# Optimization experiments

Hardware: AMD Instinct MI355X
Metric: run time of the kernel (lower is better)

Reference implementation:

```python
import jax, jax.numpy as jnp
import numpy as np

HIDDEN = 1024
NUM_HEADS = 16
HEAD_DIM = HIDDEN // NUM_HEADS
GRID_SIZE = 5
SPLINE_ORDER = 3
NUM_COEF = GRID_SIZE + SPLINE_ORDER  # 8


def make_grid(in_features):
    # efficient-kan default grid: range [-1, 1], extended by spline_order on each side
    h = 2.0 / GRID_SIZE
    g = jnp.arange(-SPLINE_ORDER, GRID_SIZE + SPLINE_ORDER + 1, dtype=jnp.float32) * h - 1.0
    return jnp.broadcast_to(g, (in_features, g.shape[0]))  # (in, G+2k+1)


def b_splines(x, grid):
    # x: (N, in); grid: (in, G+2k+1) -> bases (N, in, G+k)
    x = x[..., None]
    bases = ((x >= grid[:, :-1]) & (x < grid[:, 1:])).astype(x.dtype)
    for k in range(1, SPLINE_ORDER + 1):
        left = (x - grid[:, : -(k + 1)]) / (grid[:, k:-1] - grid[:, : -(k + 1)])
        right = (grid[:, k + 1 :] - x) / (grid[:, k + 1 :] - grid[:, 1:-k])
        bases = left * bases[..., :-1] + right * bases[..., 1:]
    return bases


def kan_linear(x, base_w, spline_w, spline_scaler):
    # x: (..., in); base_w: (out, in); spline_w: (out, in, C); spline_scaler: (out, in)
    in_f = x.shape[-1]
    x2 = x.reshape(-1, in_f)
    base = jax.nn.silu(x2) @ base_w.T
    bases = b_splines(x2, make_grid(in_f))                      # (N, in, C)
    sw = spline_w * spline_scaler[..., None]                    # (out, in, C)
    spline = bases.reshape(x2.shape[0], -1) @ sw.reshape(sw.shape[0], -1).T
    return (base + spline).reshape(*x.shape[:-1], base_w.shape[0])


def apply_rope(x):
    # x: (B, H, S, D); interleaved rotary (lucidrains convention), theta=10000
    d, s = x.shape[-1], x.shape[-2]
    inv_freq = 1.0 / (10000.0 ** (jnp.arange(0, d, 2, dtype=jnp.float32) / d))
    freqs = jnp.arange(s, dtype=jnp.float32)[:, None] * inv_freq[None, :]  # (S, d/2)
    cos = jnp.repeat(jnp.cos(freqs), 2, axis=-1)
    sin = jnp.repeat(jnp.sin(freqs), 2, axis=-1)
    x1, x2 = x[..., 0::2], x[..., 1::2]
    rot = jnp.stack((-x2, x1), axis=-1).reshape(x.shape)
    return x * cos + rot * sin


def setup_inputs() -> dict:
    key = jax.random.key(0)
    ks = jax.random.split(key, 10)
    B, S, H = 2, 2048, HIDDEN
    H3 = 3 * H
    scale = 0.02
    return {
        "q": jax.random.normal(ks[0], (B, S, H), jnp.float32),
        "k": jax.random.normal(ks[1], (B, S, H), jnp.float32),
        "v": jax.random.normal(ks[2], (B, S, H), jnp.float32),
        "attn_mask": jnp.zeros((S, S), jnp.float32),
        "qkv_base_w": jax.random.normal(ks[3], (H3, H3), jnp.float32) * scale,
        "qkv_spline_w": jax.random.normal(ks[4], (H3, H3, NUM_COEF), jnp.float32) * scale,
        "qkv_scaler": jnp.ones((H3, H3), jnp.float32),
        "out_base_w": jax.random.normal(ks[5], (H, H), jnp.float32) * scale,
        "out_spline_w": jax.random.normal(ks[6], (H, H, NUM_COEF), jnp.float32) * scale,
        "out_scaler": jnp.ones((H, H), jnp.float32),
    }


def reference(q, k, v, attn_mask, qkv_base_w, qkv_spline_w, qkv_scaler,
              out_base_w, out_spline_w, out_scaler):
    B, S, H = q.shape
    x = jnp.concatenate((q, k, v), axis=2)                       # (B, S, 3H)
    qkv = kan_linear(x, qkv_base_w, qkv_spline_w, qkv_scaler)    # (B, S, 3H)
    qkv = qkv.reshape(B, S, NUM_HEADS, 3 * HEAD_DIM).transpose(0, 2, 1, 3)
    queries, keys, values = jnp.split(qkv, 3, axis=-1)           # each (B, nh, S, hd)
    queries = apply_rope(queries)
    keys = apply_rope(keys)
    scores = jnp.einsum("bhqd,bhkd->bhqk", queries, keys) / (HEAD_DIM ** 0.5) + attn_mask
    attention = jax.nn.softmax(scores, axis=-1)
    context = jnp.einsum("bhqk,bhkd->bhqd", attention, values)
    context = context.transpose(0, 2, 1, 3).reshape(B, S, H)
    return kan_linear(context, out_base_w, out_spline_w, out_scaler)
```

## Files before the change

### kernel.cpp

```cpp
#include <hip/hip_runtime.h>
#include <hip/hip_bf16.h>
#include <stdint.h>

typedef __bf16 bf16;
typedef __attribute__((ext_vector_type(4))) __bf16 bf16x4;
typedef __attribute__((ext_vector_type(8))) __bf16 bf16x8;
typedef __attribute__((ext_vector_type(4))) float f32x4;

#define DEVI __device__ __forceinline__

constexpr int BATCH = 2, SEQ = 2048, HID = 1024, NHEAD = 16, HDIM = 64;
constexpr int H3 = 3072;
constexpr int MROWS = BATCH * SEQ;
constexpr int KEXP = 9;
constexpr int K1DIM = H3 * KEXP;
constexpr int K2DIM = HID * KEXP;

constexpr size_t WQ_OFF  = 0;
constexpr size_t AQ_OFF  = 169869312;
constexpr size_t CQ_OFF  = AQ_OFF + 226492416;
constexpr size_t QR_OFF  = CQ_OFF + 50331648;
constexpr size_t KR_OFF  = QR_OFF + 8388608;
constexpr size_t VB_OFF  = KR_OFF + 8388608;
constexpr size_t CTX_OFF = VB_OFF + 8388608;
constexpr size_t A2_OFF  = 0;
constexpr size_t W2_OFF  = 75497472;
constexpr size_t MB_OFF  = W2_OFF + 18874368;

DEVI void gld_lds16(const void* g, void* l) {
  __builtin_amdgcn_global_load_lds((const __attribute__((address_space(1))) void*)g,
                                   (__attribute__((address_space(3))) void*)l, 16, 0, 0);
}

#define WAITVM0() asm volatile("s_waitcnt vmcnt(0)" ::: "memory")
#define MEMFENCE() asm volatile("" ::: "memory")
#define BARRIER() do { __builtin_amdgcn_s_barrier(); asm volatile("" ::: "memory"); } while (0)

DEVI void silu_bases(float x, float* o9) {
  o9[0] = x / (1.0f + __expf(-x));
  float g[12];
#pragma unroll
  for (int j = 0; j < 12; ++j) g[j] = (float)(j - 3) * 0.4f - 1.0f;
  float b[11];
#pragma unroll
  for (int j = 0; j < 11; ++j) b[j] = (x >= g[j] && x < g[j + 1]) ? 1.0f : 0.0f;
#pragma unroll
  for (int k = 1; k <= 3; ++k) {
    const float inv = (k == 1) ? 2.5f : (k == 2) ? 1.25f : (1.0f / 1.2f);
#pragma unroll
    for (int j = 0; j + k < 11; ++j) {
      b[j] = (x - g[j]) * inv * b[j] + (g[j + k + 1] - x) * inv * b[j + 1];
    }
  }
#pragma unroll
  for (int c = 0; c < 8; ++c) o9[1 + c] = b[c];
}

__global__ __launch_bounds__(256)
void wprep_kernel(const float* __restrict__ bw, const float* __restrict__ sw,
                  const float* __restrict__ sc, bf16* __restrict__ W, int KK) {
  __shared__ bf16 buf[256 * KEXP];
  const int tid = threadIdx.x;
  const int n = blockIdx.y;
  const int i0 = blockIdx.x * 256;
  const size_t idx = (size_t)n * KK + i0 + tid;
  float base = bw[idx];
  float scal = sc[idx];
  const float4* sp = (const float4*)(sw + idx * 8);
  float4 s0 = sp[0], s1 = sp[1];
  bf16* o = buf + tid * KEXP;
  o[0] = (bf16)base;
  o[1] = (bf16)(s0.x * scal); o[2] = (bf16)(s0.y * scal);
  o[3] = (bf16)(s0.z * scal); o[4] = (bf16)(s0.w * scal);
  o[5] = (bf16)(s1.x * scal); o[6] = (bf16)(s1.y * scal);
  o[7] = (bf16)(s1.z * scal); o[8] = (bf16)(s1.w * scal);
  __syncthreads();
  bf16* dst = W + (size_t)n * KK * KEXP + (size_t)i0 * KEXP;
#pragma unroll
  for (int j = tid; j < 256 * KEXP / 8; j += 256)
    *(bf16x8*)(dst + j * 8) = *(const bf16x8*)(buf + j * 8);
}

__global__ __launch_bounds__(256)
void act_qkv_kernel(const float* __restrict__ qin, const float* __restrict__ kin,
                    const float* __restrict__ vin, bf16* __restrict__ A) {
  __shared__ bf16 buf[256 * KEXP];
  const int tid = threadIdx.x;
  const int m = blockIdx.y;
  const int i0 = blockIdx.x * 256;
  const int i = i0 + tid;
  const int which = i >> 10, off = i & 1023;
  const float* src = (which == 0) ? qin : (which == 1) ? kin : vin;
  float x = src[(size_t)m * HID + off];
  float o9[9];
  silu_bases(x, o9);
  bf16* o = buf + tid * KEXP;
#pragma unroll
  for (int c = 0; c < 9; ++c) o[c] = (bf16)o9[c];
  __syncthreads();
  bf16* dst = A + (size_t)m * K1DIM + (size_t)i0 * KEXP;
#pragma unroll
  for (int j = tid; j < 256 * KEXP / 8; j += 256)
    *(bf16x8*)(dst + j * 8) = *(const bf16x8*)(buf + j * 8);
}

__global__ __launch_bounds__(256)
void act_out_kernel(const float* __restrict__ ctx, bf16* __restrict__ A) {
  __shared__ bf16 buf[256 * KEXP];
  const int tid = threadIdx.x;
  const int m = blockIdx.y;
  const int i0 = blockIdx.x * 256;
  float x = ctx[(size_t)m * HID + i0 + tid];
  float o9[9];
  silu_bases(x, o9);
  bf16* o = buf + tid * KEXP;
#pragma unroll
  for (int c = 0; c < 9; ++c) o[c] = (bf16)o9[c];
  __syncthreads();
  bf16* dst = A + (size_t)m * K2DIM + (size_t)i0 * KEXP;
#pragma unroll
  for (int j = tid; j < 256 * KEXP / 8; j += 256)
    *(bf16x8*)(dst + j * 8) = *(const bf16x8*)(buf + j * 8);
}

__global__ __launch_bounds__(256)
void maskprep_kernel(const float* __restrict__ m, bf16* __restrict__ mb) {
  int i = (blockIdx.x * 256 + threadIdx.x) * 4;
  float4 v = *(const float4*)(m + i);
  bf16x4 o = { (bf16)v.x, (bf16)v.y, (bf16)v.z, (bf16)v.w };
  *(bf16x4*)(mb + i) = o;
}

__global__ __launch_bounds__(256, 2)
void gemm_kernel(const bf16* __restrict__ A, const bf16* __restrict__ Bw,
                 float* __restrict__ C, int N, int K) {
  __shared__ bf16 As[128 * 64];
  __shared__ bf16 Bs[128 * 64];
  const int tid = threadIdx.x;
  const int lane = tid & 63;
  const int l15 = lane & 15, lq = lane >> 4;
  const int wid = tid >> 6;
  const int wm = (wid >> 1) * 64, wn = (wid & 1) * 64;
  const int bm = blockIdx.y, bn = blockIdx.x;
  f32x4 acc[4][4] = {};
  const int srow = tid >> 3;
  const int schk = (tid & 7) ^ (srow & 7);
  const bf16* aB = A + (size_t)(bm * 128 + srow) * K + schk * 8;
  const bf16* bB = Bw + (size_t)(bn * 128 + srow) * K + schk * 8;

  int aoff[2][4], boff[2][4];
#pragma unroll
  for (int ks = 0; ks < 2; ++ks) {
#pragma unroll
    for (int f = 0; f < 4; ++f) {
      int arow = wm + f * 16 + l15;
      int brow = wn + f * 16 + l15;
      aoff[ks][f] = arow * 64 + (((ks * 4 + lq) ^ (arow & 7)) * 8);
      boff[ks][f] = brow * 64 + (((ks * 4 + lq) ^ (brow & 7)) * 8);
    }
  }

  for (int kt = 0; kt < K; kt += 64) {
#pragma unroll
    for (int r = 0; r < 4; ++r) {
      gld_lds16(aB + (size_t)(r * 32) * K + kt, As + r * 2048 + tid * 8);
      gld_lds16(bB + (size_t)(r * 32) * K + kt, Bs + r * 2048 + tid * 8);
    }
    __syncthreads();
#pragma unroll
    for (int ks = 0; ks < 2; ++ks) {
      bf16x8 af[4], bfr[4];
#pragma unroll
      for (int mf = 0; mf < 4; ++mf)
        af[mf] = *(const bf16x8*)&As[aoff[ks][mf]];
#pragma unroll
      for (int nf = 0; nf < 4; ++nf)
        bfr[nf] = *(const bf16x8*)&Bs[boff[ks][nf]];
#pragma unroll
      for (int mf = 0; mf < 4; ++mf)
#pragma unroll
        for (int nf = 0; nf < 4; ++nf)
          acc[mf][nf] = __builtin_amdgcn_mfma_f32_16x16x32_bf16(af[mf], bfr[nf], acc[mf][nf], 0, 0, 0);
    }
    __syncthreads();
  }
#pragma unroll
  for (int mf = 0; mf < 4; ++mf)
#pragma unroll
    for (int nf = 0; nf < 4; ++nf)
#pragma unroll
      for (int r = 0; r < 4; ++r) {
        int row = bm * 128 + wm + mf * 16 + lq * 4 + r;
        int col = bn * 128 + wn + nf * 16 + l15;
        C[(size_t)row * N + col] = acc[mf][nf][r];
      }
}

__global__ __launch_bounds__(256, 2)
void gemm2_kernel(const bf16* __restrict__ A, const bf16* __restrict__ Bw,
                  float* __restrict__ C, int N, int K) {
  __shared__ bf16 As[64 * 64];
  __shared__ bf16 Bs[128 * 64];
  const int tid = threadIdx.x;
  const int lane = tid & 63;
  const int l15 = lane & 15, lq = lane >> 4;
  const int wid = tid >> 6;
  const int wr = wid >> 1, wc = wid & 1;
  const int bm = blockIdx.y, bn = blockIdx.x;
  f32x4 acc[2][4] = {};
  const int srow = tid >> 3;
  const int schk = (tid & 7) ^ (srow & 7);
  const bf16* aB = A + (size_t)(bm * 64 + srow) * K + schk * 8;
  const bf16* bB = Bw + (size_t)(bn * 128 + srow) * K + schk * 8;

  int aoff[2][2], boff[2][4];
#pragma unroll
  for (int ks = 0; ks < 2; ++ks) {
#pragma unroll
    for (int f = 0; f < 2; ++f) {
      int arow = wr * 32 + f * 16 + l15;
      aoff[ks][f] = arow * 64 + (((ks * 4 + lq) ^ (arow & 7)) * 8);
    }
#pragma unroll
    for (int f = 0; f < 4; ++f) {
      int brow = wc * 64 + f * 16 + l15;
      boff[ks][f] = brow * 64 + (((ks * 4 + lq) ^ (brow & 7)) * 8);
    }
  }

  for (int kt = 0; kt < K; kt += 64) {
#pragma unroll
    for (int r = 0; r < 2; ++r)
      gld_lds16(aB + (size_t)(r * 32) * K + kt, As + r * 2048 + tid * 8);
#pragma unroll
    for (int r = 0; r < 4; ++r)
      gld_lds16(bB + (size_t)(r * 32) * K + kt, Bs + r * 2048 + tid * 8);
    __syncthreads();
#pragma unroll
    for (int ks = 0; ks < 2; ++ks) {
      bf16x8 af[2], bfr[4];
#pragma unroll
      for (int mf = 0; mf < 2; ++mf)
        af[mf] = *(const bf16x8*)&As[aoff[ks][mf]];
#pragma unroll
      for (int nf = 0; nf < 4; ++nf)
        bfr[nf] = *(const bf16x8*)&Bs[boff[ks][nf]];
#pragma unroll
      for (int mf = 0; mf < 2; ++mf)
#pragma unroll
        for (int nf = 0; nf < 4; ++nf)
          acc[mf][nf] = __builtin_amdgcn_mfma_f32_16x16x32_bf16(af[mf], bfr[nf], acc[mf][nf], 0, 0, 0);
    }
    __syncthreads();
  }
#pragma unroll
  for (int mf = 0; mf < 2; ++mf)
#pragma unroll
    for (int nf = 0; nf < 4; ++nf)
#pragma unroll
      for (int r = 0; r < 4; ++r) {
        int row = bm * 64 + wr * 32 + mf * 16 + lq * 4 + r;
        int col = bn * 128 + wc * 64 + nf * 16 + l15;
        C[(size_t)row * N + col] = acc[mf][nf][r];
      }
}

__global__ void rope_kernel(const float* __restrict__ Cq, bf16* __restrict__ qr,
                            bf16* __restrict__ kr, bf16* __restrict__ vt) {
  int idx = blockIdx.x * blockDim.x + threadIdx.x;
  int p = idx & 31;
  int h = (idx >> 5) & 15;
  int m = idx >> 9;
  int s = m & (SEQ - 1);
  int b = m >> 11;
  const float* row = Cq + (size_t)m * H3 + h * 192;
  float q0 = row[2 * p], q1 = row[2 * p + 1];
  float k0 = row[64 + 2 * p], k1 = row[64 + 2 * p + 1];
  float v0 = row[128 + 2 * p], v1 = row[128 + 2 * p + 1];
  float invf = expf(-(float)p * (9.210340371976184f / 32.0f));
  float fr = (float)s * invf;
  float sn, cs;
  sincosf(fr, &sn, &cs);
  const int bh = b * NHEAD + h;
  size_t o = ((size_t)bh * SEQ + s) * 64 + 2 * p;
  qr[o] = (bf16)((q0 * cs - q1 * sn) * 0.125f);
  qr[o + 1] = (bf16)((q1 * cs + q0 * sn) * 0.125f);
  kr[o] = (bf16)(k0 * cs - k1 * sn); kr[o + 1] = (bf16)(k1 * cs + k0 * sn);
  vt[((size_t)bh * 64 + 2 * p) * SEQ + s] = (bf16)v0;
  vt[((size_t)bh * 64 + 2 * p + 1) * SEQ + s] = (bf16)v1;
}

__global__ __launch_bounds__(256, 2)
void attn_kernel(const bf16* __restrict__ qr, const bf16* __restrict__ kr,
                 const bf16* __restrict__ vt, const bf16* __restrict__ maskb,
                 float* __restrict__ ctx) {
  __shared__ bf16 Kt[2][64 * 64];
  __shared__ bf16 Vt[2][64 * 64];
  __shared__ bf16 Pl[4][16 * 64];
  const int tid = threadIdx.x, lane = tid & 63, wid = tid >> 6;
  const int l15 = lane & 15, lq = lane >> 4;
  const int qt = blockIdx.x, bh = blockIdx.y;
  const int b = bh >> 4, hh = bh & 15;
  const size_t baseQ = ((size_t)bh * SEQ + qt * 64 + wid * 16) * 64;
  bf16x8 aq[2];
  aq[0] = *(const bf16x8*)&qr[baseQ + (size_t)l15 * 64 + 0 + lq * 8];
  aq[1] = *(const bf16x8*)&qr[baseQ + (size_t)l15 * 64 + 32 + lq * 8];
  float mrow[4], lrow[4];
  f32x4 oacc[4] = {};
#pragma unroll
  for (int r = 0; r < 4; ++r) { mrow[r] = -1e30f; lrow[r] = 0.0f; }
  const int srow = tid >> 3;
  const int schk = (tid & 7) ^ (srow & 7);
  const bf16* kBase = kr + ((size_t)bh * SEQ + srow) * 64 + schk * 8;
  const bf16* vBase = vt + ((size_t)bh * 64 + srow) * SEQ + schk * 8;

#define ASTAGE(bi_, kv_)                                                        \
  do {                                                                          \
    gld_lds16(kBase + (size_t)(kv_) * 64, &Kt[bi_][0] + tid * 8);               \
    gld_lds16(kBase + (size_t)((kv_) + 32) * 64, &Kt[bi_][0] + 2048 + tid * 8); \
    gld_lds16(vBase + (kv_), &Vt[bi_][0] + tid * 8);                            \
    gld_lds16(vBase + (size_t)32 * SEQ + (kv_), &Vt[bi_][0] + 2048 + tid * 8);  \
  } while (0)

  ASTAGE(0, 0);
  WAITVM0();
  BARRIER();
  for (int kv0 = 0; kv0 < SEQ; kv0 += 64) {
    const int cur = (kv0 >> 6) & 1;
    if (kv0 + 64 < SEQ) { ASTAGE(cur ^ 1, kv0 + 64); MEMFENCE(); }
    const bf16* kt = &Kt[cur][0];
    const bf16* vtl = &Vt[cur][0];
    f32x4 sacc[4] = {};
    __builtin_amdgcn_s_setprio(1);
#pragma unroll
    for (int k0 = 0; k0 < 2; ++k0) {
#pragma unroll
      for (int nf = 0; nf < 4; ++nf) {
        bf16x8 bk = *(const bf16x8*)&kt[(nf * 16 + l15) * 64 + (((k0 * 4 + lq) ^ (l15 & 7)) << 3)];
        sacc[nf] = __builtin_amdgcn_mfma_f32_16x16x32_bf16(aq[k0], bk, sacc[nf], 0, 0, 0);
      }
    }
    __builtin_amdgcn_s_setprio(0);
    const int qg0 = qt * 64 + wid * 16 + lq * 4;
#pragma unroll
    for (int nf = 0; nf < 4; ++nf) {
      int kvg = kv0 + nf * 16 + l15;
#pragma unroll
      for (int r = 0; r < 4; ++r)
        sacc[nf][r] += (float)maskb[(size_t)(qg0 + r) * SEQ + kvg];
    }
    float fac[4];
#pragma unroll
    for (int r = 0; r < 4; ++r) {
      float v = fmaxf(fmaxf(sacc[0][r], sacc[1][r]), fmaxf(sacc[2][r], sacc[3][r]));
      v = fmaxf(v, __shfl_xor(v, 1));
      v = fmaxf(v, __shfl_xor(v, 2));
      v = fmaxf(v, __shfl_xor(v, 4));
      v = fmaxf(v, __shfl_xor(v, 8));
      float mnew = fmaxf(mrow[r], v);
      fac[r] = __expf(mrow[r] - mnew);
      mrow[r] = mnew;
    }
    float rs[4] = {0, 0, 0, 0};
#pragma unroll
    for (int nf = 0; nf < 4; ++nf)
#pragma unroll
      for (int r = 0; r < 4; ++r) {
        float pv = __expf(sacc[nf][r] - mrow[r]);
        sacc[nf][r] = pv;
        rs[r] += pv;
      }
#pragma unroll
    for (int r = 0; r < 4; ++r) {
      float v = rs[r];
      v += __shfl_xor(v, 1); v += __shfl_xor(v, 2);
      v += __shfl_xor(v, 4); v += __shfl_xor(v, 8);
      lrow[r] = lrow[r] * fac[r] + v;
    }
#pragma unroll
    for (int nf = 0; nf < 4; ++nf)
#pragma unroll
      for (int r = 0; r < 4; ++r) {
        int qrow = lq * 4 + r;
        int col = nf * 16 + l15;
        Pl[wid][qrow * 64 + ((((col >> 3) ^ (qrow & 7))) << 3) + (col & 7)] = (bf16)sacc[nf][r];
      }
#pragma unroll
    for (int nf = 0; nf < 4; ++nf)
#pragma unroll
      for (int r = 0; r < 4; ++r)
        oacc[nf][r] *= fac[r];
    __builtin_amdgcn_s_setprio(1);
#pragma unroll
    for (int k0 = 0; k0 < 2; ++k0) {
      bf16x8 ap = *(const bf16x8*)&Pl[wid][l15 * 64 + (((k0 * 4 + lq) ^ (l15 & 7)) << 3)];
#pragma unroll
      for (int nf = 0; nf < 4; ++nf) {
        bf16x8 bv = *(const bf16x8*)&vtl[(nf * 16 + l15) * 64 + (((k0 * 4 + lq) ^ (l15 & 7)) << 3)];
        oacc[nf] = __builtin_amdgcn_mfma_f32_16x16x32_bf16(ap, bv, oacc[nf], 0, 0, 0);
      }
    }
    __builtin_amdgcn_s_setprio(0);
    WAITVM0();
    BARRIER();
  }
#undef ASTAGE
#pragma unroll
  for (int nf = 0; nf < 4; ++nf)
#pragma unroll
    for (int r = 0; r < 4; ++r) {
      int row = qt * 64 + wid * 16 + lq * 4 + r;
      int col = hh * 64 + nf * 16 + l15;
      ctx[((size_t)b * SEQ + row) * HID + col] = oacc[nf][r] / lrow[r];
    }
}

extern "C" void kernel_launch(void* const* d_in, const int* in_sizes, int n_in,
                              void* d_out, int out_size, void* d_ws, size_t ws_size,
                              hipStream_t stream) {
  const float* qin    = (const float*)d_in[0];
  const float* kin    = (const float*)d_in[1];
  const float* vin    = (const float*)d_in[2];
  const float* mask   = (const float*)d_in[3];
  const float* qkv_bw = (const float*)d_in[4];
  const float* qkv_sw = (const float*)d_in[5];
  const float* qkv_sc = (const float*)d_in[6];
  const float* out_bw = (const float*)d_in[7];
  const float* out_sw = (const float*)d_in[8];
  const float* out_sc = (const float*)d_in[9];
  char* ws = (char*)d_ws;
  bf16* Wq  = (bf16*)(ws + WQ_OFF);
  bf16* Aq  = (bf16*)(ws + AQ_OFF);
  float* Cq = (float*)(ws + CQ_OFF);
  bf16* qr  = (bf16*)(ws + QR_OFF);
  bf16* kr  = (bf16*)(ws + KR_OFF);
  bf16* vt  = (bf16*)(ws + VB_OFF);
  float* ctx = (float*)(ws + CTX_OFF);
  bf16* A2  = (bf16*)(ws + A2_OFF);
  bf16* W2  = (bf16*)(ws + W2_OFF);
  bf16* mb  = (bf16*)(ws + MB_OFF);

  wprep_kernel<<<dim3(H3 / 256, H3), 256, 0, stream>>>(qkv_bw, qkv_sw, qkv_sc, Wq, H3);
  act_qkv_kernel<<<dim3(H3 / 256, MROWS), 256, 0, stream>>>(qin, kin, vin, Aq);
  gemm_kernel<<<dim3(H3 / 128, MROWS / 128), 256, 0, stream>>>(Aq, Wq, Cq, H3, K1DIM);
  maskprep_kernel<<<(SEQ * SEQ) / 1024, 256, 0, stream>>>(mask, mb);
  rope_kernel<<<(MROWS * NHEAD * 32) / 256, 256, 0, stream>>>(Cq, qr, kr, vt);
  attn_kernel<<<dim3(SEQ / 64, BATCH * NHEAD), 256, 0, stream>>>(qr, kr, vt, mb, ctx);
  act_out_kernel<<<dim3(HID / 256, MROWS), 256, 0, stream>>>(ctx, A2);
  wprep_kernel<<<dim3(HID / 256, HID), 256, 0, stream>>>(out_bw, out_sw, out_sc, W2, HID);
  gemm2_kernel<<<dim3(HID / 128, MROWS / 64), 256, 0, stream>>>(A2, W2, (float*)d_out, HID, K2DIM);
}
```

Measured before the change: 1.119 ms.

## Process two 16-row query groups per wave in attention kernel

Each wave now handles 32 query rows (two 16-row groups) instead of 16, so every block covers 128 queries and the grid halves. Each K/V tile staged in shared memory is reused for twice as many queries, which halves global K/V traffic and staging per query. In exchange, register pressure rises from the doubled accumulators and the grid has fewer blocks (512), which may lower occupancy and latency hiding. The attention kernel is only part of a pipeline dominated by large KAN GEMMs.

```diff
diff --git a/kernel.cpp b/kernel.cpp
--- a/kernel.cpp
+++ b/kernel.cpp
@@ -296,19 +296,24 @@
                  float* __restrict__ ctx) {
   __shared__ bf16 Kt[2][64 * 64];
   __shared__ bf16 Vt[2][64 * 64];
-  __shared__ bf16 Pl[4][16 * 64];
+  __shared__ bf16 Pl[4][32 * 64];
   const int tid = threadIdx.x, lane = tid & 63, wid = tid >> 6;
   const int l15 = lane & 15, lq = lane >> 4;
   const int qt = blockIdx.x, bh = blockIdx.y;
   const int b = bh >> 4, hh = bh & 15;
-  const size_t baseQ = ((size_t)bh * SEQ + qt * 64 + wid * 16) * 64;
-  bf16x8 aq[2];
-  aq[0] = *(const bf16x8*)&qr[baseQ + (size_t)l15 * 64 + 0 + lq * 8];
-  aq[1] = *(const bf16x8*)&qr[baseQ + (size_t)l15 * 64 + 32 + lq * 8];
-  float mrow[4], lrow[4];
-  f32x4 oacc[4] = {};
-#pragma unroll
-  for (int r = 0; r < 4; ++r) { mrow[r] = -1e30f; lrow[r] = 0.0f; }
+  bf16x8 aq[2][2];
+#pragma unroll
+  for (int g = 0; g < 2; ++g) {
+    const size_t baseQ = ((size_t)bh * SEQ + qt * 128 + wid * 32 + g * 16) * 64;
+    aq[g][0] = *(const bf16x8*)&qr[baseQ + (size_t)l15 * 64 + 0 + lq * 8];
+    aq[g][1] = *(const bf16x8*)&qr[baseQ + (size_t)l15 * 64 + 32 + lq * 8];
+  }
+  float mrow[2][4], lrow[2][4];
+  f32x4 oacc[2][4] = {};
+#pragma unroll
+  for (int g = 0; g < 2; ++g)
+#pragma unroll
+    for (int r = 0; r < 4; ++r) { mrow[g][r] = -1e30f; lrow[g][r] = 0.0f; }
   const int srow = tid >> 3;
   const int schk = (tid & 7) ^ (srow & 7);
   const bf16* kBase = kr + ((size_t)bh * SEQ + srow) * 64 + schk * 8;
@@ -330,74 +335,82 @@
     if (kv0 + 64 < SEQ) { ASTAGE(cur ^ 1, kv0 + 64); MEMFENCE(); }
     const bf16* kt = &Kt[cur][0];
     const bf16* vtl = &Vt[cur][0];
-    f32x4 sacc[4] = {};
+    f32x4 sacc[2][4] = {};
     __builtin_amdgcn_s_setprio(1);
 #pragma unroll
     for (int k0 = 0; k0 < 2; ++k0) {
 #pragma unroll
       for (int nf = 0; nf < 4; ++nf) {
         bf16x8 bk = *(const bf16x8*)&kt[(nf * 16 + l15) * 64 + (((k0 * 4 + lq) ^ (l15 & 7)) << 3)];
-        sacc[nf] = __builtin_amdgcn_mfma_f32_16x16x32_bf16(aq[k0], bk, sacc[nf], 0, 0, 0);
+#pragma unroll
+        for (int g = 0; g < 2; ++g)
+          sacc[g][nf] = __builtin_amdgcn_mfma_f32_16x16x32_bf16(aq[g][k0], bk, sacc[g][nf], 0, 0, 0);
       }
     }
     __builtin_amdgcn_s_setprio(0);
-    const int qg0 = qt * 64 + wid * 16 + lq * 4;
-#pragma unroll
-    for (int nf = 0; nf < 4; ++nf) {
-      int kvg = kv0 + nf * 16 + l15;
-#pragma unroll
-      for (int r = 0; r < 4; ++r)
-        sacc[nf][r] += (float)maskb[(size_t)(qg0 + r) * SEQ + kvg];
-    }
-    float fac[4];
-#pragma unroll
-    for (int r = 0; r < 4; ++r) {
-      float v = fmaxf(fmaxf(sacc[0][r], sacc[1][r]), fmaxf(sacc[2][r], sacc[3][r]));
-      v = fmaxf(v, __shfl_xor(v, 1));
-      v = fmaxf(v, __shfl_xor(v, 2));
-      v = fmaxf(v, __shfl_xor(v, 4));
-      v = fmaxf(v, __shfl_xor(v, 8));
-      float mnew = fmaxf(mrow[r], v);
-      fac[r] = __expf(mrow[r] - mnew);
-      mrow[r] = mnew;
-    }
-    float rs[4] = {0, 0, 0, 0};
-#pragma unroll
-    for (int nf = 0; nf < 4; ++nf)
+#pragma unroll
+    for (int g = 0; g < 2; ++g) {
+      const int qg0 = qt * 128 + wid * 32 + g * 16 + lq * 4;
+#pragma unroll
+      for (int nf = 0; nf < 4; ++nf) {
+        int kvg = kv0 + nf * 16 + l15;
+#pragma unroll
+        for (int r = 0; r < 4; ++r)
+          sacc[g][nf][r] += (float)maskb[(size_t)(qg0 + r) * SEQ + kvg];
+      }
+      float fac[4];
 #pragma unroll
       for (int r = 0; r < 4; ++r) {
-        float pv = __expf(sacc[nf][r] - mrow[r]);
-        sacc[nf][r] = pv;
-        rs[r] += pv;
-      }
-#pragma unroll
-    for (int r = 0; r < 4; ++r) {
-      float v = rs[r];
-      v += __shfl_xor(v, 1); v += __shfl_xor(v, 2);
-      v += __shfl_xor(v, 4); v += __shfl_xor(v, 8);
-      lrow[r] = lrow[r] * fac[r] + v;
-    }
-#pragma unroll
-    for (int nf = 0; nf < 4; ++nf)
+        float v = fmaxf(fmaxf(sacc[g][0][r], sacc[g][1][r]), fmaxf(sacc[g][2][r], sacc[g][3][r]));
+        v = fmaxf(v, __shfl_xor(v, 1));
+        v = fmaxf(v, __shfl_xor(v, 2));
+        v = fmaxf(v, __shfl_xor(v, 4));
+        v = fmaxf(v, __shfl_xor(v, 8));
+        float mnew = fmaxf(mrow[g][r], v);
+        fac[r] = __expf(mrow[g][r] - mnew);
+        mrow[g][r] = mnew;
+      }
+      float rs[4] = {0, 0, 0, 0};
+#pragma unroll
+      for (int nf = 0; nf < 4; ++nf)
+#pragma unroll
+        for (int r = 0; r < 4; ++r) {
+          float pv = __expf(sacc[g][nf][r] - mrow[g][r]);
+          sacc[g][nf][r] = pv;
+          rs[r] += pv;
+        }
 #pragma unroll
       for (int r = 0; r < 4; ++r) {
-        int qrow = lq * 4 + r;
-        int col = nf * 16 + l15;
-        Pl[wid][qrow * 64 + ((((col >> 3) ^ (qrow & 7))) << 3) + (col & 7)] = (bf16)sacc[nf][r];
-      }
-#pragma unroll
-    for (int nf = 0; nf < 4; ++nf)
-#pragma unroll
-      for (int r = 0; r < 4; ++r)
-        oacc[nf][r] *= fac[r];
+        float v = rs[r];
+        v += __shfl_xor(v, 1); v += __shfl_xor(v, 2);
+        v += __shfl_xor(v, 4); v += __shfl_xor(v, 8);
+        lrow[g][r] = lrow[g][r] * fac[r] + v;
+      }
+#pragma unroll
+      for (int nf = 0; nf < 4; ++nf)
+#pragma unroll
+        for (int r = 0; r < 4; ++r) {
+          int qrow = g * 16 + lq * 4 + r;
+          int col = nf * 16 + l15;
+          Pl[wid][qrow * 64 + ((((col >> 3) ^ (qrow & 7))) << 3) + (col & 7)] = (bf16)sacc[g][nf][r];
+        }
+#pragma unroll
+      for (int nf = 0; nf < 4; ++nf)
+#pragma unroll
+        for (int r = 0; r < 4; ++r)
+          oacc[g][nf][r] *= fac[r];
+    }
     __builtin_amdgcn_s_setprio(1);
 #pragma unroll
     for (int k0 = 0; k0 < 2; ++k0) {
-      bf16x8 ap = *(const bf16x8*)&Pl[wid][l15 * 64 + (((k0 * 4 + lq) ^ (l15 & 7)) << 3)];
-#pragma unroll
-      for (int nf = 0; nf < 4; ++nf) {
-        bf16x8 bv = *(const bf16x8*)&vtl[(nf * 16 + l15) * 64 + (((k0 * 4 + lq) ^ (l15 & 7)) << 3)];
-        oacc[nf] = __builtin_amdgcn_mfma_f32_16x16x32_bf16(ap, bv, oacc[nf], 0, 0, 0);
+#pragma unroll
+      for (int g = 0; g < 2; ++g) {
+        bf16x8 ap = *(const bf16x8*)&Pl[wid][(g * 16 + l15) * 64 + (((k0 * 4 + lq) ^ (l15 & 7)) << 3)];
+#pragma unroll
+        for (int nf = 0; nf < 4; ++nf) {
+          bf16x8 bv = *(const bf16x8*)&vtl[(nf * 16 + l15) * 64 + (((k0 * 4 + lq) ^ (l15 & 7)) << 3)];
+          oacc[g][nf] = __builtin_amdgcn_mfma_f32_16x16x32_bf16(ap, bv, oacc[g][nf], 0, 0, 0);
+        }
       }
     }
     __builtin_amdgcn_s_setprio(0);
@@ -406,13 +419,15 @@
   }
 #undef ASTAGE
 #pragma unroll
-  for (int nf = 0; nf < 4; ++nf)
-#pragma unroll
-    for (int r = 0; r < 4; ++r) {
-      int row = qt * 64 + wid * 16 + lq * 4 + r;
-      int col = hh * 64 + nf * 16 + l15;
-      ctx[((size_t)b * SEQ + row) * HID + col] = oacc[nf][r] / lrow[r];
-    }
+  for (int g = 0; g < 2; ++g)
+#pragma unroll
+    for (int nf = 0; nf < 4; ++nf)
+#pragma unroll
+      for (int r = 0; r < 4; ++r) {
+        int row = qt * 128 + wid * 32 + g * 16 + lq * 4 + r;
+        int col = hh * 64 + nf * 16 + l15;
+        ctx[((size_t)b * SEQ + row) * HID + col] = oacc[g][nf][r] / lrow[g][r];
+      }
 }
 
 extern "C" void kernel_launch(void* const* d_in, const int* in_sizes, int n_in,
@@ -445,7 +460,7 @@
   gemm_kernel<<<dim3(H3 / 128, MROWS / 128), 256, 0, stream>>>(Aq, Wq, Cq, H3, K1DIM);
   maskprep_kernel<<<(SEQ * SEQ) / 1024, 256, 0, stream>>>(mask, mb);
   rope_kernel<<<(MROWS * NHEAD * 32) / 256, 256, 0, stream>>>(Cq, qr, kr, vt);
-  attn_kernel<<<dim3(SEQ / 64, BATCH * NHEAD), 256, 0, stream>>>(qr, kr, vt, mb, ctx);
+  attn_kernel<<<dim3(SEQ / 128, BATCH * NHEAD), 256, 0, stream>>>(qr, kr, vt, mb, ctx);
   act_out_kernel<<<dim3(HID / 256, MROWS), 256, 0, stream>>>(ctx, A2);
   wprep_kernel<<<dim3(HID / 256, HID), 256, 0, stream>>>(out_bw, out_sw, out_sc, W2, HID);
   gemm2_kernel<<<dim3(HID / 128, MROWS / 64), 256, 0, stream>>>(A2, W2, (float*)d_out, HID, K2DIM);
```

New measurement: 1.204 ms. 1.08x slower.

## Fuse RoPE and head split into QKV GEMM epilogue, add V transpose kernel

Applied to the files above, without the earlier changes.

The QKV GEMM epilogue now applies rotary embedding and writes bf16 q/k (q pre-scaled) and a row-major bf16 V directly, using a precomputed cos/sin table and a lane shuffle to fetch the paired element. A separate small kernel transposes V through LDS into the layout attention expects. This removes the 50MB fp32 intermediate write and readback plus the strided scatter in the old rope kernel. In exchange it adds per-element index math and scattered 2-byte stores in the epilogue, and two extra small launches.

```diff
diff --git a/kernel.cpp b/kernel.cpp
--- a/kernel.cpp
+++ b/kernel.cpp
@@ -19,6 +19,8 @@
 constexpr size_t WQ_OFF  = 0;
 constexpr size_t AQ_OFF  = 169869312;
 constexpr size_t CQ_OFF  = AQ_OFF + 226492416;
+constexpr size_t VR_OFF  = CQ_OFF;
+constexpr size_t TC_OFF  = CQ_OFF + 16777216;
 constexpr size_t QR_OFF  = CQ_OFF + 50331648;
 constexpr size_t KR_OFF  = QR_OFF + 8388608;
 constexpr size_t VB_OFF  = KR_OFF + 8388608;
@@ -54,6 +56,16 @@
   }
 #pragma unroll
   for (int c = 0; c < 8; ++c) o9[1 + c] = b[c];
+}
+
+__global__ __launch_bounds__(256)
+void tprep_kernel(float2* __restrict__ tcs) {
+  int idx = blockIdx.x * 256 + threadIdx.x;
+  int s = idx >> 5, p = idx & 31;
+  float invf = __expf(-(float)p * (9.210340371976184f / 32.0f));
+  float sn, cs;
+  __sincosf((float)s * invf, &sn, &cs);
+  tcs[idx] = make_float2(cs, sn);
 }
 
 __global__ __launch_bounds__(256)
@@ -132,8 +144,9 @@
 }
 
 __global__ __launch_bounds__(256, 2)
-void gemm_kernel(const bf16* __restrict__ A, const bf16* __restrict__ Bw,
-                 float* __restrict__ C, int N, int K) {
+void gemm1_kernel(const bf16* __restrict__ A, const bf16* __restrict__ Bw,
+                  bf16* __restrict__ qr, bf16* __restrict__ kr,
+                  bf16* __restrict__ vrow, const float2* __restrict__ tcs, int K) {
   __shared__ bf16 As[128 * 64];
   __shared__ bf16 Bs[128 * 64];
   const int tid = threadIdx.x;
@@ -184,16 +197,56 @@
     }
     __syncthreads();
   }
+
 #pragma unroll
   for (int mf = 0; mf < 4; ++mf)
 #pragma unroll
     for (int nf = 0; nf < 4; ++nf)
 #pragma unroll
-      for (int r = 0; r < 4; ++r) {
-        int row = bm * 128 + wm + mf * 16 + lq * 4 + r;
+      for (int rr = 0; rr < 4; ++rr) {
+        int row = bm * 128 + wm + mf * 16 + lq * 4 + rr;
         int col = bn * 128 + wn + nf * 16 + l15;
-        C[(size_t)row * N + col] = acc[mf][nf][r];
-      }
+        int s = row & (SEQ - 1);
+        int bb = row >> 11;
+        int h = col / 192;
+        int r2 = col - h * 192;
+        int bh = bb * NHEAD + h;
+        float val = acc[mf][nf][rr];
+        float par = __shfl_xor(val, 1);
+        if (r2 < 128) {
+          int d = r2 & 63;
+          float2 cz = tcs[s * 32 + (d >> 1)];
+          float o = (col & 1) ? (val * cz.x + par * cz.y)
+                              : (val * cz.x - par * cz.y);
+          if (r2 < 64) qr[((size_t)bh * SEQ + s) * 64 + d] = (bf16)(o * 0.125f);
+          else         kr[((size_t)bh * SEQ + s) * 64 + d] = (bf16)o;
+        } else {
+          vrow[((size_t)bh * SEQ + s) * 64 + (r2 - 128)] = (bf16)val;
+        }
+      }
+}
+
+__global__ __launch_bounds__(256)
+void vtrans_kernel(const bf16* __restrict__ vrow, bf16* __restrict__ vt) {
+  __shared__ bf16 t[64][72];
+  const int tid = threadIdx.x;
+  const int st = blockIdx.x, bh = blockIdx.y;
+  const size_t base = ((size_t)bh * SEQ + st * 64) * 64;
+#pragma unroll
+  for (int r = 0; r < 2; ++r) {
+    int row = r * 32 + (tid >> 3);
+    int c8 = (tid & 7) * 8;
+    *(bf16x8*)&t[row][c8] = *(const bf16x8*)&vrow[base + (size_t)row * 64 + c8];
+  }
+  __syncthreads();
+  const int d = tid >> 2;
+  const int s0 = (tid & 3) * 16;
+  bf16 tmp[16];
+#pragma unroll
+  for (int e = 0; e < 16; ++e) tmp[e] = t[s0 + e][d];
+  bf16* dst = vt + ((size_t)(bh * 64 + d)) * SEQ + st * 64 + s0;
+  *(bf16x8*)dst = *(bf16x8*)&tmp[0];
+  *(bf16x8*)(dst + 8) = *(bf16x8*)&tmp[8];
 }
 
 __global__ __launch_bounds__(256, 2)
@@ -263,31 +316,6 @@
         int col = bn * 128 + wc * 64 + nf * 16 + l15;
         C[(size_t)row * N + col] = acc[mf][nf][r];
       }
-}
-
-__global__ void rope_kernel(const float* __restrict__ Cq, bf16* __restrict__ qr,
-                            bf16* __restrict__ kr, bf16* __restrict__ vt) {
-  int idx = blockIdx.x * blockDim.x + threadIdx.x;
-  int p = idx & 31;
-  int h = (idx >> 5) & 15;
-  int m = idx >> 9;
-  int s = m & (SEQ - 1);
-  int b = m >> 11;
-  const float* row = Cq + (size_t)m * H3 + h * 192;
-  float q0 = row[2 * p], q1 = row[2 * p + 1];
-  float k0 = row[64 + 2 * p], k1 = row[64 + 2 * p + 1];
-  float v0 = row[128 + 2 * p], v1 = row[128 + 2 * p + 1];
-  float invf = expf(-(float)p * (9.210340371976184f / 32.0f));
-  float fr = (float)s * invf;
-  float sn, cs;
-  sincosf(fr, &sn, &cs);
-  const int bh = b * NHEAD + h;
-  size_t o = ((size_t)bh * SEQ + s) * 64 + 2 * p;
-  qr[o] = (bf16)((q0 * cs - q1 * sn) * 0.125f);
-  qr[o + 1] = (bf16)((q1 * cs + q0 * sn) * 0.125f);
-  kr[o] = (bf16)(k0 * cs - k1 * sn); kr[o + 1] = (bf16)(k1 * cs + k0 * sn);
-  vt[((size_t)bh * 64 + 2 * p) * SEQ + s] = (bf16)v0;
-  vt[((size_t)bh * 64 + 2 * p + 1) * SEQ + s] = (bf16)v1;
 }
 
 __global__ __launch_bounds__(256, 2)
@@ -429,22 +457,24 @@
   const float* out_sw = (const float*)d_in[8];
   const float* out_sc = (const float*)d_in[9];
   char* ws = (char*)d_ws;
-  bf16* Wq  = (bf16*)(ws + WQ_OFF);
-  bf16* Aq  = (bf16*)(ws + AQ_OFF);
-  float* Cq = (float*)(ws + CQ_OFF);
-  bf16* qr  = (bf16*)(ws + QR_OFF);
-  bf16* kr  = (bf16*)(ws + KR_OFF);
-  bf16* vt  = (bf16*)(ws + VB_OFF);
+  bf16* Wq   = (bf16*)(ws + WQ_OFF);
+  bf16* Aq   = (bf16*)(ws + AQ_OFF);
+  bf16* vrow = (bf16*)(ws + VR_OFF);
+  float2* tcs = (float2*)(ws + TC_OFF);
+  bf16* qr   = (bf16*)(ws + QR_OFF);
+  bf16* kr   = (bf16*)(ws + KR_OFF);
+  bf16* vt   = (bf16*)(ws + VB_OFF);
   float* ctx = (float*)(ws + CTX_OFF);
-  bf16* A2  = (bf16*)(ws + A2_OFF);
-  bf16* W2  = (bf16*)(ws + W2_OFF);
-  bf16* mb  = (bf16*)(ws + MB_OFF);
-
+  bf16* A2   = (bf16*)(ws + A2_OFF);
+  bf16* W2   = (bf16*)(ws + W2_OFF);
+  bf16* mb   = (bf16*)(ws + MB_OFF);
+
+  tprep_kernel<<<256, 256, 0, stream>>>(tcs);
   wprep_kernel<<<dim3(H3 / 256, H3), 256, 0, stream>>>(qkv_bw, qkv_sw, qkv_sc, Wq, H3);
   act_qkv_kernel<<<dim3(H3 / 256, MROWS), 256, 0, stream>>>(qin, kin, vin, Aq);
-  gemm_kernel<<<dim3(H3 / 128, MROWS / 128), 256, 0, stream>>>(Aq, Wq, Cq, H3, K1DIM);
+  gemm1_kernel<<<dim3(H3 / 128, MROWS / 128), 256, 0, stream>>>(Aq, Wq, qr, kr, vrow, tcs, K1DIM);
   maskprep_kernel<<<(SEQ * SEQ) / 1024, 256, 0, stream>>>(mask, mb);
-  rope_kernel<<<(MROWS * NHEAD * 32) / 256, 256, 0, stream>>>(Cq, qr, kr, vt);
+  vtrans_kernel<<<dim3(SEQ / 64, BATCH * NHEAD), 256, 0, stream>>>(vrow, vt);
   attn_kernel<<<dim3(SEQ / 64, BATCH * NHEAD), 256, 0, stream>>>(qr, kr, vt, mb, ctx);
   act_out_kernel<<<dim3(HID / 256, MROWS), 256, 0, stream>>>(ctx, A2);
   wprep_kernel<<<dim3(HID / 256, HID), 256, 0, stream>>>(out_bw, out_sw, out_sc, W2, HID);
```

Result: no change. 1.120 ms, median of 2 (+0.1%).
